# Kernel optimization log

Measured on AMD Instinct MI355X. Metric: run time of the kernel, lower is better.

## Reference

```python
import jax, jax.numpy as jnp
import numpy as np

N_EMB = 1024
N_HEAD = 16
HD = N_EMB // N_HEAD
ROPE_BASE = 10000.0


def _rope_cos_sin(seq_len, dim, dtype):
    inv_freq = 1.0 / (ROPE_BASE ** (jnp.arange(0, dim, 2, dtype=jnp.float32) / dim))
    t = jnp.arange(seq_len, dtype=jnp.float32)
    freqs = jnp.outer(t, inv_freq)              # [S, dim/2]
    emb = jnp.concatenate([freqs, freqs], -1)    # [S, dim]
    return jnp.cos(emb).astype(dtype), jnp.sin(emb).astype(dtype)


def _rotate_half(x):
    x1, x2 = jnp.split(x, 2, axis=-1)
    return jnp.concatenate([-x2, x1], axis=-1)


def _apply_rope(x):
    # x: [B, H, L, hd]; rotary over sequence axis (-2)
    cos, sin = _rope_cos_sin(x.shape[-2], x.shape[-1], x.dtype)
    return x * cos + _rotate_half(x) * sin


def setup_inputs() -> dict:
    key = jax.random.key(0)
    ks = jax.random.split(key, 8)
    B, T, S = 2, 2048, 2048
    std = 0.02
    return {
        "x": jax.random.normal(ks[0], (B, T, N_EMB), jnp.float32),
        "memory": jax.random.normal(ks[1], (B, S, N_EMB), jnp.float32),
        "q_w": jax.random.normal(ks[2], (N_EMB, N_EMB), jnp.float32) * std,
        "q_b": jnp.zeros((N_EMB,), jnp.float32),
        "kv_w": jax.random.normal(ks[3], (N_EMB, 2 * N_EMB), jnp.float32) * std,
        "kv_b": jnp.zeros((2 * N_EMB,), jnp.float32),
        "proj_w": jax.random.normal(ks[4], (N_EMB, N_EMB), jnp.float32) * std,
        "proj_b": jnp.zeros((N_EMB,), jnp.float32),
    }


def reference(x, memory, q_w, q_b, kv_w, kv_b, proj_w, proj_b):
    B, S, C = memory.shape
    T = x.shape[1]
    kv = memory @ kv_w + kv_b                      # [B,S,2C]
    K, V = jnp.split(kv, 2, axis=-1)
    Q = x @ q_w + q_b                              # [B,T,C]

    def heads(t, L):
        return t.reshape(B, L, N_HEAD, HD).transpose(0, 2, 1, 3)

    Q, K, V = heads(Q, T), heads(K, S), heads(V, S)
    Q = jax.nn.elu(Q) + 1.0                        # positive feature map
    K = jax.nn.elu(K) + 1.0
    Q_rot = _apply_rope(Q)
    K_rot = _apply_rope(K)
    # denom row-sum: sum_s Q.K_s == Q . (sum_s K_s) -- identical math, no SxT matrix
    denom = jnp.einsum('bhtd,bhd->bht', Q, K.sum(axis=2))[..., None]  # [B,H,T,1]
    att = jnp.einsum('bhtd,bhsd->bhts', Q_rot, K_rot) / denom          # [B,H,T,S]
    y = jnp.einsum('bhts,bhsd->bhtd', att, V)                          # [B,H,T,hd]
    y = y.transpose(0, 2, 1, 3).reshape(B, T, C)
    return y @ proj_w + proj_b
```

## Files before the change

kernel.cpp:

```cpp
#include <hip/hip_runtime.h>
#include <cstddef>
#include <cstdint>

#define B_SZ  2
#define T_SEQ 2048
#define S_SEQ 2048
#define C_EMB 1024
#define NH    16
#define HD    64
#define KDIM  1024

typedef __attribute__((ext_vector_type(8))) short bf16x8;
typedef __attribute__((ext_vector_type(4))) float f32x4;

#define OFF_XH    ((size_t)0)
#define OFF_XL    ((size_t)2097152)
#define OFF_MEMH  ((size_t)4194304)
#define OFF_MEML  ((size_t)6291456)
#define OFF_QWH   ((size_t)8388608)
#define OFF_QWL   ((size_t)8912896)
#define OFF_KVWH  ((size_t)9437184)
#define OFF_KVWL  ((size_t)10485760)
#define OFF_PWH   ((size_t)11534336)
#define OFF_PWL   ((size_t)12058624)
#define OFF_KSUM  ((size_t)12582912)
#define OFF_MT    ((size_t)12584960)
#define OFF_TAB   ((size_t)12716032)
#define OFF_YH    ((size_t)12847104)
#define OFF_YL    ((size_t)14944256)
#define WS_FLOATS ((size_t)17041408)

__device__ __forceinline__ float elu1(float v) {
    return v > 0.0f ? v + 1.0f : __expf(v);
}
__device__ __forceinline__ unsigned short bf16_rne(float x) {
    union { float f; unsigned int u; } v; v.f = x;
    unsigned int u = v.u;
    return (unsigned short)((u + 0x7FFFu + ((u >> 16) & 1u)) >> 16);
}
__device__ __forceinline__ float bf16_to_f(unsigned short h) {
    union { unsigned int u; float f; } v; v.u = ((unsigned int)h) << 16;
    return v.f;
}

#define PREP_BLOCKS 13064

__device__ __forceinline__ void split4_body(
    const float4* __restrict__ in, ushort4* __restrict__ hi,
    ushort4* __restrict__ lo, int i)
{
    float4 v = in[i];
    ushort4 h, l;
    h.x = bf16_rne(v.x); l.x = bf16_rne(v.x - bf16_to_f(h.x));
    h.y = bf16_rne(v.y); l.y = bf16_rne(v.y - bf16_to_f(h.y));
    h.z = bf16_rne(v.z); l.z = bf16_rne(v.z - bf16_to_f(h.z));
    h.w = bf16_rne(v.w); l.w = bf16_rne(v.w - bf16_to_f(h.w));
    hi[i] = h; lo[i] = l;
}

__device__ __forceinline__ void transpose_body(
    const float* __restrict__ W, unsigned short* __restrict__ Wth,
    unsigned short* __restrict__ Wtl, int K, int N, int bx, int by,
    float (*tile)[33])
{
    const int k0 = by * 32, n0 = bx * 32;
    const int tx = threadIdx.x & 31, ty = threadIdx.x >> 5;
    #pragma unroll
    for (int j = 0; j < 4; ++j)
        tile[ty + j * 8][tx] = W[(size_t)(k0 + ty + j * 8) * N + n0 + tx];
    __syncthreads();
    #pragma unroll
    for (int j = 0; j < 4; ++j) {
        float x = tile[tx][ty + j * 8];
        unsigned short h = bf16_rne(x);
        unsigned short l = bf16_rne(x - bf16_to_f(h));
        size_t o = (size_t)(n0 + ty + j * 8) * K + k0 + tx;
        Wth[o] = h; Wtl[o] = l;
    }
}

__global__ __launch_bounds__(256) void prep_kernel(
    const float* __restrict__ x, const float* __restrict__ memory,
    const float* __restrict__ q_w, const float* __restrict__ kv_w,
    const float* __restrict__ proj_w,
    unsigned short* __restrict__ xh, unsigned short* __restrict__ xl,
    unsigned short* __restrict__ mh, unsigned short* __restrict__ ml,
    unsigned short* __restrict__ qwh, unsigned short* __restrict__ qwl,
    unsigned short* __restrict__ kvwh, unsigned short* __restrict__ kvwl,
    unsigned short* __restrict__ pwh, unsigned short* __restrict__ pwl,
    float2* __restrict__ tab, float* __restrict__ zero_base)
{
    __shared__ float tile[32][33];
    const int bid = blockIdx.x;
    const int tid = threadIdx.x;
    if (bid < 4096) {
        split4_body((const float4*)x, (ushort4*)xh, (ushort4*)xl, bid * 256 + tid);
    } else if (bid < 8192) {
        split4_body((const float4*)memory, (ushort4*)mh, (ushort4*)ml, (bid - 4096) * 256 + tid);
    } else if (bid < 9216) {
        int i = bid - 8192;
        transpose_body(q_w, qwh, qwl, 1024, 1024, i & 31, i >> 5, tile);
    } else if (bid < 11264) {
        int i = bid - 9216;
        transpose_body(kv_w, kvwh, kvwl, 1024, 2048, i & 63, i >> 6, tile);
    } else if (bid < 12288) {
        int i = bid - 11264;
        transpose_body(proj_w, pwh, pwl, 1024, 1024, i & 31, i >> 5, tile);
    } else if (bid < 12544) {
        int idx = (bid - 12288) * 256 + tid;
        int pos = idx >> 5, i = idx & 31;
        double invf = exp(-(double)i * (9.210340371976184 / 32.0));
        float arg = (float)((double)pos * invf);
        float sn, cs;
        sincosf(arg, &sn, &cs);
        tab[idx] = make_float2(cs, sn);
    } else {
        int idx = (bid - 12544) * 256 + tid;
        if (idx < 2048 + 131072) zero_base[idx] = 0.0f;
    }
}

__device__ __forceinline__ void gemm_main_loop_64(
    const unsigned short* __restrict__ Ah, const unsigned short* __restrict__ Al,
    const unsigned short* __restrict__ Bth, const unsigned short* __restrict__ Btl,
    unsigned short* lds, int m0, int n0, f32x4 acc[2][4])
{
    const int tid = threadIdx.x;
    const int w = tid >> 6, lane = tid & 63;
    const int quad = lane >> 4, lrow = lane & 15;
    const int srow = lane >> 2;
    const int scol = (lane & 3) * 8;

    const unsigned short* src = (w == 0) ? Ah : (w == 1) ? Al : (w == 2) ? Bth : Btl;
    const int rbase = (w < 2) ? m0 : n0;
    const unsigned short* gsrc = src + (size_t)(rbase + srow) * KDIM + scol;
    unsigned short* lbase = (w < 2) ? &lds[w * 8192] : &lds[16384 + (w - 2) * 4096];

    const unsigned short* As_h = lds;
    const unsigned short* As_l = lds + 8192;
    const unsigned short* Bs_h = lds + 16384;
    const unsigned short* Bs_l = lds + 20480;

    for (int k0 = 0; k0 < KDIM; k0 += 64) {
        if (w < 2) {
            #pragma unroll
            for (int p = 0; p < 2; ++p)
                #pragma unroll
                for (int i = 0; i < 8; ++i)
                    __builtin_amdgcn_global_load_lds(
                        (const __attribute__((address_space(1))) unsigned int*)(gsrc + (size_t)i * 16 * KDIM + k0 + p * 32),
                        (__attribute__((address_space(3))) unsigned int*)(lbase + p * 4096 + i * 512),
                        16, 0, 0);
        } else {
            #pragma unroll
            for (int p = 0; p < 2; ++p)
                #pragma unroll
                for (int i = 0; i < 4; ++i)
                    __builtin_amdgcn_global_load_lds(
                        (const __attribute__((address_space(1))) unsigned int*)(gsrc + (size_t)i * 16 * KDIM + k0 + p * 32),
                        (__attribute__((address_space(3))) unsigned int*)(lbase + p * 2048 + i * 512),
                        16, 0, 0);
        }
        __syncthreads();

        #pragma unroll
        for (int p = 0; p < 2; ++p) {
            bf16x8 bh[4], bl[4];
            #pragma unroll
            for (int jt = 0; jt < 4; ++jt) {
                int nl = jt * 16 + lrow;
                bh[jt] = *(const bf16x8*)&Bs_h[p * 2048 + nl * 32 + quad * 8];
                bl[jt] = *(const bf16x8*)&Bs_l[p * 2048 + nl * 32 + quad * 8];
            }
            #pragma unroll
            for (int it = 0; it < 2; ++it) {
                int ml = w * 32 + it * 16 + lrow;
                bf16x8 ah = *(const bf16x8*)&As_h[p * 4096 + ml * 32 + quad * 8];
                bf16x8 al = *(const bf16x8*)&As_l[p * 4096 + ml * 32 + quad * 8];
                #pragma unroll
                for (int jt = 0; jt < 4; ++jt) {
                    acc[it][jt] = __builtin_amdgcn_mfma_f32_16x16x32_bf16(ah, bh[jt], acc[it][jt], 0, 0, 0);
                    acc[it][jt] = __builtin_amdgcn_mfma_f32_16x16x32_bf16(ah, bl[jt], acc[it][jt], 0, 0, 0);
                    acc[it][jt] = __builtin_amdgcn_mfma_f32_16x16x32_bf16(al, bh[jt], acc[it][jt], 0, 0, 0);
                }
            }
        }
        __syncthreads();
    }
}

__global__ __launch_bounds__(256) void gemm_kv(
    const unsigned short* __restrict__ Ah, const unsigned short* __restrict__ Al,
    const unsigned short* __restrict__ Bth, const unsigned short* __restrict__ Btl,
    const float* __restrict__ bias, const float2* __restrict__ tab,
    float* __restrict__ Ksum, float* __restrict__ Mt)
{
    __shared__ unsigned short smem[34816];
    const int tid = threadIdx.x;
    const int w = tid >> 6, lane = tid & 63;
    const int wr = w >> 1, wc = w & 1;
    const int quad = lane >> 4, lrow = lane & 15;
    const int h  = blockIdx.x;
    const int m0 = blockIdx.y * 128;
    const int b  = m0 >> 11;
    const int tbase = (m0 & 2047) + wr * 64;

    {
        const unsigned short* src = (w == 0) ? Ah : (w == 1) ? Al : (w == 2) ? Bth : Btl;
        const int srow = lane >> 2, scol = (lane & 3) * 8;
        const size_t rowbase = (w < 2) ? (size_t)(m0 + srow) : (size_t)(h * 64 + srow);
        const unsigned short* gsrc = src + rowbase * KDIM + scol;
        const size_t vskip = (w >= 2) ? (size_t)960 * KDIM : 0;
        unsigned short* lbase = &smem[w * 8192];
        const unsigned short* As_h = smem;
        const unsigned short* As_l = smem + 8192;
        const unsigned short* Bs_h = smem + 16384;
        const unsigned short* Bs_l = smem + 24576;

        f32x4 acc[4][4] = {};
        for (int k0 = 0; k0 < KDIM; k0 += 64) {
            #pragma unroll
            for (int p = 0; p < 2; ++p)
                #pragma unroll
                for (int i = 0; i < 8; ++i) {
                    size_t goff = (size_t)i * 16 * KDIM + k0 + p * 32 + ((i >= 4) ? vskip : 0);
                    __builtin_amdgcn_global_load_lds(
                        (const __attribute__((address_space(1))) unsigned int*)(gsrc + goff),
                        (__attribute__((address_space(3))) unsigned int*)(lbase + p * 4096 + i * 512),
                        16, 0, 0);
                }
            __syncthreads();
            #pragma unroll
            for (int p = 0; p < 2; ++p) {
                bf16x8 bh[4], bl[4];
                #pragma unroll
                for (int jt = 0; jt < 4; ++jt) {
                    int nl = wc * 64 + jt * 16 + lrow;
                    bh[jt] = *(const bf16x8*)&Bs_h[p * 4096 + nl * 32 + quad * 8];
                    bl[jt] = *(const bf16x8*)&Bs_l[p * 4096 + nl * 32 + quad * 8];
                }
                #pragma unroll
                for (int it = 0; it < 4; ++it) {
                    int ml = wr * 64 + it * 16 + lrow;
                    bf16x8 ah = *(const bf16x8*)&As_h[p * 4096 + ml * 32 + quad * 8];
                    bf16x8 al = *(const bf16x8*)&As_l[p * 4096 + ml * 32 + quad * 8];
                    #pragma unroll
                    for (int jt = 0; jt < 4; ++jt) {
                        acc[it][jt] = __builtin_amdgcn_mfma_f32_16x16x32_bf16(ah, bh[jt], acc[it][jt], 0, 0, 0);
                        acc[it][jt] = __builtin_amdgcn_mfma_f32_16x16x32_bf16(ah, bl[jt], acc[it][jt], 0, 0, 0);
                        acc[it][jt] = __builtin_amdgcn_mfma_f32_16x16x32_bf16(al, bh[jt], acc[it][jt], 0, 0, 0);
                    }
                }
            }
            __syncthreads();
        }

        const bool isK = (wc == 0);
        const int colg = (isK ? 0 : C_EMB) + h * 64;
        float bb[4];
        #pragma unroll
        for (int jt = 0; jt < 4; ++jt) bb[jt] = bias[colg + jt * 16 + lrow];
        #pragma unroll
        for (int it = 0; it < 4; ++it)
            #pragma unroll
            for (int jt = 0; jt < 4; ++jt)
                #pragma unroll
                for (int r = 0; r < 4; ++r) {
                    float v = acc[it][jt][r] + bb[jt];
                    acc[it][jt][r] = isK ? elu1(v) : v;
                }

        if (isK) {
            #pragma unroll
            for (int jt = 0; jt < 4; ++jt) {
                float p = 0.0f;
                #pragma unroll
                for (int it = 0; it < 4; ++it)
                    #pragma unroll
                    for (int r = 0; r < 4; ++r) p += acc[it][jt][r];
                p += __shfl_xor(p, 16);
                p += __shfl_xor(p, 32);
                if (quad == 0)
                    atomicAdd(&Ksum[b * C_EMB + h * 64 + jt * 16 + lrow], p);
            }
            #pragma unroll
            for (int it = 0; it < 4; ++it)
                #pragma unroll
                for (int r = 0; r < 4; ++r) {
                    int s = tbase + it * 16 + quad * 4 + r;
                    float2 c0 = tab[s * 32 + lrow];
                    float2 c1 = tab[s * 32 + 16 + lrow];
                    float a0 = acc[it][0][r], a1 = acc[it][1][r];
                    float a2 = acc[it][2][r], a3 = acc[it][3][r];
                    acc[it][0][r] = a0 * c0.x - a2 * c0.y;
                    acc[it][2][r] = a2 * c0.x + a0 * c0.y;
                    acc[it][1][r] = a1 * c1.x - a3 * c1.y;
                    acc[it][3][r] = a3 * c1.x + a1 * c1.y;
                }
        }

        unsigned short* Hd = smem + (isK ? 0 : 17408);
        unsigned short* Ld = Hd + 8704;
        #pragma unroll
        for (int jt = 0; jt < 4; ++jt) {
            int d = jt * 16 + lrow;
            #pragma unroll
            for (int it = 0; it < 4; ++it) {
                int t0loc = wr * 64 + it * 16 + quad * 4;
                ushort4 h4, l4;
                float v0 = acc[it][jt][0], v1 = acc[it][jt][1];
                float v2 = acc[it][jt][2], v3 = acc[it][jt][3];
                h4.x = bf16_rne(v0); l4.x = bf16_rne(v0 - bf16_to_f(h4.x));
                h4.y = bf16_rne(v1); l4.y = bf16_rne(v1 - bf16_to_f(h4.y));
                h4.z = bf16_rne(v2); l4.z = bf16_rne(v2 - bf16_to_f(h4.z));
                h4.w = bf16_rne(v3); l4.w = bf16_rne(v3 - bf16_to_f(h4.w));
                *(ushort4*)&Hd[d * 136 + t0loc] = h4;
                *(ushort4*)&Ld[d * 136 + t0loc] = l4;
            }
        }
    }
    __syncthreads();

    {
        const unsigned short* KH = smem;
        const unsigned short* KL = smem + 8704;
        const unsigned short* VH = smem + 17408;
        const unsigned short* VL = smem + 26112;
        const int mrow = w * 16 + lrow;
        f32x4 macc[4] = {};
        #pragma unroll
        for (int ks = 0; ks < 4; ++ks) {
            int kof = ks * 32 + quad * 8;
            bf16x8 vah = *(const bf16x8*)&VH[mrow * 136 + kof];
            bf16x8 val = *(const bf16x8*)&VL[mrow * 136 + kof];
            #pragma unroll
            for (int jt = 0; jt < 4; ++jt) {
                int nrow = jt * 16 + lrow;
                bf16x8 kbh = *(const bf16x8*)&KH[nrow * 136 + kof];
                bf16x8 kbl = *(const bf16x8*)&KL[nrow * 136 + kof];
                macc[jt] = __builtin_amdgcn_mfma_f32_16x16x32_bf16(vah, kbh, macc[jt], 0, 0, 0);
                macc[jt] = __builtin_amdgcn_mfma_f32_16x16x32_bf16(vah, kbl, macc[jt], 0, 0, 0);
                macc[jt] = __builtin_amdgcn_mfma_f32_16x16x32_bf16(val, kbh, macc[jt], 0, 0, 0);
            }
        }
        const int bh = b * NH + h;
        #pragma unroll
        for (int jt = 0; jt < 4; ++jt)
            #pragma unroll
            for (int r = 0; r < 4; ++r)
                atomicAdd(&Mt[((size_t)bh * 64 + w * 16 + quad * 4 + r) * 64 + jt * 16 + lrow],
                          macc[jt][r]);
    }
}

__global__ __launch_bounds__(256) void gemm_q(
    const unsigned short* __restrict__ Ah, const unsigned short* __restrict__ Al,
    const unsigned short* __restrict__ Bth, const unsigned short* __restrict__ Btl,
    const float* __restrict__ bias, const float2* __restrict__ tab,
    const float* __restrict__ Ksum, const float* __restrict__ Mt,
    unsigned short* __restrict__ Yh, unsigned short* __restrict__ Yl)
{
    __shared__ unsigned short smem[24576];
    const int h  = blockIdx.x;
    const int m0 = blockIdx.y * 128;
    f32x4 acc[2][4] = {};
    gemm_main_loop_64(Ah, Al, Bth, Btl, smem, m0, h * 64, acc);

    const int tid = threadIdx.x;
    const int w = tid >> 6, lane = tid & 63;
    const int quad = lane >> 4, lrow = lane & 15;
    const int b = m0 >> 11;
    const int tbase = (m0 & 2047) + w * 32;
    const int bh = b * NH + h;

    float bb[4];
    #pragma unroll
    for (int jt = 0; jt < 4; ++jt) bb[jt] = bias[h * 64 + jt * 16 + lrow];
    #pragma unroll
    for (int it = 0; it < 2; ++it)
        #pragma unroll
        for (int jt = 0; jt < 4; ++jt)
            #pragma unroll
            for (int r = 0; r < 4; ++r)
                acc[it][jt][r] = elu1(acc[it][jt][r] + bb[jt]);

    float ks[4], den_reg[2][4];
    #pragma unroll
    for (int jt = 0; jt < 4; ++jt) ks[jt] = Ksum[b * C_EMB + h * 64 + jt * 16 + lrow];
    #pragma unroll
    for (int it = 0; it < 2; ++it)
        #pragma unroll
        for (int r = 0; r < 4; ++r) {
            float p = acc[it][0][r] * ks[0] + acc[it][1][r] * ks[1]
                    + acc[it][2][r] * ks[2] + acc[it][3][r] * ks[3];
            p += __shfl_xor(p, 1);
            p += __shfl_xor(p, 2);
            p += __shfl_xor(p, 4);
            p += __shfl_xor(p, 8);
            den_reg[it][r] = p;
        }

    #pragma unroll
    for (int it = 0; it < 2; ++it)
        #pragma unroll
        for (int r = 0; r < 4; ++r) {
            int s = tbase + it * 16 + quad * 4 + r;
            float2 c0 = tab[s * 32 + lrow];
            float2 c1 = tab[s * 32 + 16 + lrow];
            float a0 = acc[it][0][r], a1 = acc[it][1][r];
            float a2 = acc[it][2][r], a3 = acc[it][3][r];
            acc[it][0][r] = a0 * c0.x - a2 * c0.y;
            acc[it][2][r] = a2 * c0.x + a0 * c0.y;
            acc[it][1][r] = a1 * c1.x - a3 * c1.y;
            acc[it][3][r] = a3 * c1.x + a1 * c1.y;
        }

    unsigned short* QH = smem + w * 4608;
    unsigned short* QL = QH + 2304;
    #pragma unroll
    for (int it = 0; it < 2; ++it)
        #pragma unroll
        for (int jt = 0; jt < 4; ++jt)
            #pragma unroll
            for (int r = 0; r < 4; ++r) {
                int tloc = it * 16 + quad * 4 + r;
                int d = jt * 16 + lrow;
                float v = acc[it][jt][r];
                unsigned short hh = bf16_rne(v);
                QH[tloc * 72 + d] = hh;
                QL[tloc * 72 + d] = bf16_rne(v - bf16_to_f(hh));
            }

    f32x4 acc2[2][4] = {};
    #pragma unroll
    for (int kc = 0; kc < 2; ++kc) {
        bf16x8 mbh[4], mbl[4];
        #pragma unroll
        for (int jt2 = 0; jt2 < 4; ++jt2) {
            const float* mp = &Mt[((size_t)bh * 64 + jt2 * 16 + lrow) * 64 + kc * 32 + quad * 8];
            #pragma unroll
            for (int e = 0; e < 8; ++e) {
                float x = mp[e];
                unsigned short hh = bf16_rne(x);
                mbh[jt2][e] = (short)hh;
                mbl[jt2][e] = (short)bf16_rne(x - bf16_to_f(hh));
            }
        }
        #pragma unroll
        for (int it2 = 0; it2 < 2; ++it2) {
            int ro = (it2 * 16 + lrow) * 72 + kc * 32 + quad * 8;
            bf16x8 qh = *(const bf16x8*)&QH[ro];
            bf16x8 ql = *(const bf16x8*)&QL[ro];
            #pragma unroll
            for (int jt2 = 0; jt2 < 4; ++jt2) {
                acc2[it2][jt2] = __builtin_amdgcn_mfma_f32_16x16x32_bf16(qh, mbh[jt2], acc2[it2][jt2], 0, 0, 0);
                acc2[it2][jt2] = __builtin_amdgcn_mfma_f32_16x16x32_bf16(qh, mbl[jt2], acc2[it2][jt2], 0, 0, 0);
                acc2[it2][jt2] = __builtin_amdgcn_mfma_f32_16x16x32_bf16(ql, mbh[jt2], acc2[it2][jt2], 0, 0, 0);
            }
        }
    }

    #pragma unroll
    for (int it2 = 0; it2 < 2; ++it2)
        #pragma unroll
        for (int jt2 = 0; jt2 < 4; ++jt2)
            #pragma unroll
            for (int r = 0; r < 4; ++r) {
                float v = acc2[it2][jt2][r] / den_reg[it2][r];
                size_t o = ((size_t)(m0 + w * 32 + it2 * 16 + quad * 4 + r)) * C_EMB
                         + h * 64 + jt2 * 16 + lrow;
                unsigned short hh = bf16_rne(v);
                Yh[o] = hh;
                Yl[o] = bf16_rne(v - bf16_to_f(hh));
            }
}

__global__ __launch_bounds__(256) void gemm_out(
    const unsigned short* __restrict__ Ah, const unsigned short* __restrict__ Al,
    const unsigned short* __restrict__ Bth, const unsigned short* __restrict__ Btl,
    const float* __restrict__ bias, float* __restrict__ out)
{
    __shared__ unsigned short lds[24576];
    const int m0 = blockIdx.y * 128, n0 = blockIdx.x * 64;
    f32x4 acc[2][4] = {};
    gemm_main_loop_64(Ah, Al, Bth, Btl, lds, m0, n0, acc);

    const int tid = threadIdx.x;
    const int w = tid >> 6, lane = tid & 63;
    const int quad = lane >> 4, lrow = lane & 15;

    #pragma unroll
    for (int jt = 0; jt < 4; ++jt) {
        int gc = n0 + jt * 16 + lrow;
        float bb = bias[gc];
        #pragma unroll
        for (int it = 0; it < 2; ++it) {
            int grb = m0 + w * 32 + it * 16 + quad * 4;
            #pragma unroll
            for (int r = 0; r < 4; ++r)
                out[(size_t)(grb + r) * C_EMB + gc] = acc[it][jt][r] + bb;
        }
    }
}

extern "C" void kernel_launch(void* const* d_in, const int* in_sizes, int n_in,
                              void* d_out, int out_size, void* d_ws, size_t ws_size,
                              hipStream_t stream)
{
    const float* x      = (const float*)d_in[0];
    const float* memory = (const float*)d_in[1];
    const float* q_w    = (const float*)d_in[2];
    const float* q_b    = (const float*)d_in[3];
    const float* kv_w   = (const float*)d_in[4];
    const float* kv_b   = (const float*)d_in[5];
    const float* proj_w = (const float*)d_in[6];
    const float* proj_b = (const float*)d_in[7];

    if (ws_size < WS_FLOATS * sizeof(float)) return;

    float* ws = (float*)d_ws;
    unsigned short* xh   = (unsigned short*)(ws + OFF_XH);
    unsigned short* xl   = (unsigned short*)(ws + OFF_XL);
    unsigned short* mh   = (unsigned short*)(ws + OFF_MEMH);
    unsigned short* ml   = (unsigned short*)(ws + OFF_MEML);
    unsigned short* qwh  = (unsigned short*)(ws + OFF_QWH);
    unsigned short* qwl  = (unsigned short*)(ws + OFF_QWL);
    unsigned short* kvwh = (unsigned short*)(ws + OFF_KVWH);
    unsigned short* kvwl = (unsigned short*)(ws + OFF_KVWL);
    unsigned short* pwh  = (unsigned short*)(ws + OFF_PWH);
    unsigned short* pwl  = (unsigned short*)(ws + OFF_PWL);
    unsigned short* Yh   = (unsigned short*)(ws + OFF_YH);
    unsigned short* Yl   = (unsigned short*)(ws + OFF_YL);
    float*  Ksum = ws + OFF_KSUM;
    float*  Mm   = ws + OFF_MT;
    float2* tab  = (float2*)(ws + OFF_TAB);

    prep_kernel<<<PREP_BLOCKS, 256, 0, stream>>>(
        x, memory, q_w, kv_w, proj_w,
        xh, xl, mh, ml, qwh, qwl, kvwh, kvwl, pwh, pwl,
        tab, Ksum );

    gemm_kv<<<dim3(16, 32), 256, 0, stream>>>(mh, ml, kvwh, kvwl, kv_b, tab, Ksum, Mm);
    gemm_q<<<dim3(16, 32), 256, 0, stream>>>(xh, xl, qwh, qwl, q_b, tab, Ksum, Mm, Yh, Yl);
    gemm_out<<<dim3(16, 32), 256, 0, stream>>>(Yh, Yl, pwh, pwl, proj_b, (float*)d_out);
}
```

Baseline: 239.3 us.

## Use split-K 128x128 tiles with atomic accumulation for output projection

The output projection GEMM moves from 128x64 tiles over the full K to 128x128 tiles with K split in two across a z grid dimension. Partial results are accumulated into the output with atomicAdd, so the prep kernel now pre-fills the output with the bias. The aim is more data reuse per tile while keeping the same 512 blocks. The cost is atomic traffic, non-deterministic float summation order, and more LDS per block.

```diff
diff --git a/kernel.cpp b/kernel.cpp
--- a/kernel.cpp
+++ b/kernel.cpp
@@ -43,7 +43,7 @@
     return v.f;
 }
 
-#define PREP_BLOCKS 13064
+#define PREP_BLOCKS 17160
 
 __device__ __forceinline__ void split4_body(
     const float4* __restrict__ in, ushort4* __restrict__ hi,
@@ -82,13 +82,14 @@
 __global__ __launch_bounds__(256) void prep_kernel(
     const float* __restrict__ x, const float* __restrict__ memory,
     const float* __restrict__ q_w, const float* __restrict__ kv_w,
-    const float* __restrict__ proj_w,
+    const float* __restrict__ proj_w, const float* __restrict__ proj_b,
     unsigned short* __restrict__ xh, unsigned short* __restrict__ xl,
     unsigned short* __restrict__ mh, unsigned short* __restrict__ ml,
     unsigned short* __restrict__ qwh, unsigned short* __restrict__ qwl,
     unsigned short* __restrict__ kvwh, unsigned short* __restrict__ kvwl,
     unsigned short* __restrict__ pwh, unsigned short* __restrict__ pwl,
-    float2* __restrict__ tab, float* __restrict__ zero_base)
+    float2* __restrict__ tab, float* __restrict__ zero_base,
+    float* __restrict__ outp)
 {
     __shared__ float tile[32][33];
     const int bid = blockIdx.x;
@@ -114,9 +115,12 @@
         float sn, cs;
         sincosf(arg, &sn, &cs);
         tab[idx] = make_float2(cs, sn);
-    } else {
+    } else if (bid < 13064) {
         int idx = (bid - 12544) * 256 + tid;
         if (idx < 2048 + 131072) zero_base[idx] = 0.0f;
+    } else {
+        int f = (bid - 13064) * 256 + tid;
+        ((float4*)outp)[f] = ((const float4*)proj_b)[f & 255];
     }
 }
 
@@ -478,27 +482,72 @@
 __global__ __launch_bounds__(256) void gemm_out(
     const unsigned short* __restrict__ Ah, const unsigned short* __restrict__ Al,
     const unsigned short* __restrict__ Bth, const unsigned short* __restrict__ Btl,
-    const float* __restrict__ bias, float* __restrict__ out)
-{
-    __shared__ unsigned short lds[24576];
-    const int m0 = blockIdx.y * 128, n0 = blockIdx.x * 64;
-    f32x4 acc[2][4] = {};
-    gemm_main_loop_64(Ah, Al, Bth, Btl, lds, m0, n0, acc);
-
+    float* __restrict__ out)
+{
+    __shared__ unsigned short smem[32768];
     const int tid = threadIdx.x;
     const int w = tid >> 6, lane = tid & 63;
+    const int wr = w >> 1, wc = w & 1;
     const int quad = lane >> 4, lrow = lane & 15;
+    const int n0 = blockIdx.x * 128;
+    const int m0 = blockIdx.y * 128;
+    const int kb = blockIdx.z * 512;
+
+    const unsigned short* src = (w == 0) ? Ah : (w == 1) ? Al : (w == 2) ? Bth : Btl;
+    const int srow = lane >> 2, scol = (lane & 3) * 8;
+    const size_t rowbase = (w < 2) ? (size_t)(m0 + srow) : (size_t)(n0 + srow);
+    const unsigned short* gsrc = src + rowbase * KDIM + scol + kb;
+    unsigned short* lbase = &smem[w * 8192];
+    const unsigned short* As_h = smem;
+    const unsigned short* As_l = smem + 8192;
+    const unsigned short* Bs_h = smem + 16384;
+    const unsigned short* Bs_l = smem + 24576;
+
+    f32x4 acc[4][4] = {};
+    for (int k0 = 0; k0 < 512; k0 += 64) {
+        #pragma unroll
+        for (int p = 0; p < 2; ++p)
+            #pragma unroll
+            for (int i = 0; i < 8; ++i)
+                __builtin_amdgcn_global_load_lds(
+                    (const __attribute__((address_space(1))) unsigned int*)(gsrc + (size_t)i * 16 * KDIM + k0 + p * 32),
+                    (__attribute__((address_space(3))) unsigned int*)(lbase + p * 4096 + i * 512),
+                    16, 0, 0);
+        __syncthreads();
+        #pragma unroll
+        for (int p = 0; p < 2; ++p) {
+            bf16x8 bh[4], bl[4];
+            #pragma unroll
+            for (int jt = 0; jt < 4; ++jt) {
+                int nl = wc * 64 + jt * 16 + lrow;
+                bh[jt] = *(const bf16x8*)&Bs_h[p * 4096 + nl * 32 + quad * 8];
+                bl[jt] = *(const bf16x8*)&Bs_l[p * 4096 + nl * 32 + quad * 8];
+            }
+            #pragma unroll
+            for (int it = 0; it < 4; ++it) {
+                int ml = wr * 64 + it * 16 + lrow;
+                bf16x8 ah = *(const bf16x8*)&As_h[p * 4096 + ml * 32 + quad * 8];
+                bf16x8 al = *(const bf16x8*)&As_l[p * 4096 + ml * 32 + quad * 8];
+                #pragma unroll
+                for (int jt = 0; jt < 4; ++jt) {
+                    acc[it][jt] = __builtin_amdgcn_mfma_f32_16x16x32_bf16(ah, bh[jt], acc[it][jt], 0, 0, 0);
+                    acc[it][jt] = __builtin_amdgcn_mfma_f32_16x16x32_bf16(ah, bl[jt], acc[it][jt], 0, 0, 0);
+                    acc[it][jt] = __builtin_amdgcn_mfma_f32_16x16x32_bf16(al, bh[jt], acc[it][jt], 0, 0, 0);
+                }
+            }
+        }
+        __syncthreads();
+    }
 
     #pragma unroll
     for (int jt = 0; jt < 4; ++jt) {
-        int gc = n0 + jt * 16 + lrow;
-        float bb = bias[gc];
-        #pragma unroll
-        for (int it = 0; it < 2; ++it) {
-            int grb = m0 + w * 32 + it * 16 + quad * 4;
+        int gc = n0 + wc * 64 + jt * 16 + lrow;
+        #pragma unroll
+        for (int it = 0; it < 4; ++it) {
+            int grb = m0 + wr * 64 + it * 16 + quad * 4;
             #pragma unroll
             for (int r = 0; r < 4; ++r)
-                out[(size_t)(grb + r) * C_EMB + gc] = acc[it][jt][r] + bb;
+                atomicAdd(&out[(size_t)(grb + r) * C_EMB + gc], acc[it][jt][r]);
         }
     }
 }
@@ -536,11 +585,11 @@
     float2* tab  = (float2*)(ws + OFF_TAB);
 
     prep_kernel<<<PREP_BLOCKS, 256, 0, stream>>>(
-        x, memory, q_w, kv_w, proj_w,
+        x, memory, q_w, kv_w, proj_w, proj_b,
         xh, xl, mh, ml, qwh, qwl, kvwh, kvwl, pwh, pwl,
-        tab, Ksum );
+        tab, Ksum , (float*)d_out);
 
     gemm_kv<<<dim3(16, 32), 256, 0, stream>>>(mh, ml, kvwh, kvwl, kv_b, tab, Ksum, Mm);
     gemm_q<<<dim3(16, 32), 256, 0, stream>>>(xh, xl, qwh, qwl, q_b, tab, Ksum, Mm, Yh, Yl);
-    gemm_out<<<dim3(16, 32), 256, 0, stream>>>(Yh, Yl, pwh, pwl, proj_b, (float*)d_out);
-}
+    gemm_out<<<dim3(8, 32, 2), 256, 0, stream>>>(Yh, Yl, pwh, pwl, (float*)d_out);
+}
```

After: 251.8 us. +5.2%, slower.
